# Kernel optimization log

Hardware: AMD Instinct MI355X
Metric: run time of the kernel (lower is better)

Reference implementation:

```python
import jax, jax.numpy as jnp
import numpy as np

B, H, S, D = 4, 16, 1024, 64

def setup_inputs() -> dict:
    key = jax.random.key(0)
    kq, kk, kv, kb, km = jax.random.split(key, 5)
    return {
        "q": jax.random.normal(kq, (B, H, S, D), dtype=jnp.float32),
        "k": jax.random.normal(kk, (B, H, S, D), dtype=jnp.float32),
        "v": jax.random.normal(kv, (B, H, S, D), dtype=jnp.float32),
        "add_attn": jax.random.normal(kb, (B, 1, S, S), dtype=jnp.float32),
        "mask": jax.random.randint(km, (B, 1, 1, S), 0, 2, dtype=jnp.int32),
    }

def reference(q, k, v, add_attn, mask):
    d_emb = q.shape[-1]
    scale = 1.0 / jnp.sqrt(jnp.float32(d_emb)).astype(q.dtype)
    # scores: [B,H,Sq,Sk]
    attn = jnp.einsum('bhqd,bhkd->bhqk', q * scale, k)
    attn = attn + add_attn
    attn = jnp.where(mask == 0, jnp.asarray(-1e9, attn.dtype), attn)
    attn = jax.nn.softmax(attn, axis=-1)  # dropout with p=0 is identity
    output = jnp.einsum('bhqk,bhkd->bhqd', attn, v)
    return (output, attn)
```

## Files before the change

kernel.cpp:

```cpp
#include <hip/hip_runtime.h>
#include <math.h>

#define BB 4
#define HH 16
#define SS 1024
#define DD 64
#define QT 16
#define NKW 4
#define KPW 256
#define HPB 4
#define PTL 264
#define OSTR 68

typedef __attribute__((ext_vector_type(8))) short bf16x8;
typedef __attribute__((ext_vector_type(4))) float f32x4;
typedef __attribute__((ext_vector_type(4))) int   i32x4;

static __device__ inline unsigned short f2bf(float f) {
    unsigned int u = __float_as_uint(f);
    u += 0x7fff + ((u >> 16) & 1);
    return (unsigned short)(u >> 16);
}

__global__ __launch_bounds__(256) void convert_qk(const float* __restrict__ q,
                                                  const float* __restrict__ k,
                                                  unsigned short* __restrict__ qb,
                                                  unsigned short* __restrict__ kb) {
    const int idx = blockIdx.x * 256 + threadIdx.x;
    float4 qv = ((const float4*)q)[idx];
    float4 kv = ((const float4*)k)[idx];
    ushort4 qo = make_ushort4(f2bf(qv.x), f2bf(qv.y), f2bf(qv.z), f2bf(qv.w));
    ushort4 ko = make_ushort4(f2bf(kv.x), f2bf(kv.y), f2bf(kv.z), f2bf(kv.w));
    ((ushort4*)qb)[idx] = qo;
    ((ushort4*)kb)[idx] = ko;
}

__global__ __launch_bounds__(256) void transpose_v(const float* __restrict__ v,
                                                   unsigned short* __restrict__ vt) {
    __shared__ unsigned short t[DD][258];
    const int bh = blockIdx.y;
    const int k0 = blockIdx.x * 256;
    const float* vb = v + ((size_t)bh * SS + k0) * DD;
#pragma unroll
    for (int j = 0; j < 16; ++j) {
        const int f   = j * 256 + threadIdx.x;
        const int row = f >> 4;
        const int d4  = (f & 15) << 2;
        float4 x = ((const float4*)vb)[f];
        t[d4 + 0][row] = f2bf(x.x);
        t[d4 + 1][row] = f2bf(x.y);
        t[d4 + 2][row] = f2bf(x.z);
        t[d4 + 3][row] = f2bf(x.w);
    }
    __syncthreads();
    unsigned short* vo = vt + (size_t)bh * DD * SS + k0;
#pragma unroll
    for (int j = 0; j < 8; ++j) {
        const int f  = j * 256 + threadIdx.x;
        const int d  = f >> 5;
        const int k8 = (f & 31) << 3;
        const unsigned int* lp = (const unsigned int*)&t[d][k8];
        uint4 w;
        w.x = lp[0]; w.y = lp[1]; w.z = lp[2]; w.w = lp[3];
        *(uint4*)(vo + (size_t)d * SS + k8) = w;
    }
}

__global__ __launch_bounds__(256, 2) void attn_mfma(
    const unsigned short* __restrict__ qb,
    const unsigned short* __restrict__ kb,
    const unsigned short* __restrict__ vtb,
    const float* __restrict__ add_attn,
    const int*   __restrict__ mask,
    float* __restrict__ out,
    float* __restrict__ attn_out)
{
    const int P    = blockIdx.x;
    const int xcd  = P & 7;
    const int slot = P >> 3;
    const int hg   = slot & 3;
    const int g    = ((slot >> 2) << 3) | xcd;
    const int qt   = g & 63;
    const int b    = g >> 6;

    const int tid  = threadIdx.x;
    const int wave = tid >> 6;
    const int lane = tid & 63;
    const int col  = lane & 15;
    const int quad = lane >> 4;

    __shared__ unsigned short p_tile[NKW][QT][PTL];
    __shared__ float red_m[NKW][QT];
    __shared__ float red_l[NKW][QT];
    float* o_w = (float*)&p_tile[wave][0][0];

    const int q0  = qt * QT;
    const int wk0 = wave * KPW;

    const float* brow = add_attn + ((size_t)b * SS + q0 + col) * SS;
    const int*   mrow = mask + b * SS;
    float br[16][4];
#pragma unroll
    for (int t = 0; t < 16; ++t) {
        const int kof = wk0 + t * 16 + quad * 4;
        const f32x4 bv = *(const f32x4*)(brow + kof);
        const i32x4 mv = *(const i32x4*)(mrow + kof);
#pragma unroll
        for (int r = 0; r < 4; ++r)
            br[t][r] = mv[r] ? bv[r] : -1e9f;
    }

    for (int hi = 0; hi < HPB; ++hi) {
        const int bh = b * HH + hg * HPB + hi;

        const unsigned short* qrow = qb + ((size_t)bh * SS + q0 + col) * DD + quad * 8;
        const bf16x8 bq0 = *(const bf16x8*)(qrow);
        const bf16x8 bq1 = *(const bf16x8*)(qrow + 32);

        const unsigned short* kbb = kb + (size_t)bh * SS * DD;

        float s[16][4];
#pragma unroll
        for (int t = 0; t < 16; ++t) {
            const unsigned short* kr = kbb + (size_t)(wk0 + t * 16 + col) * DD + quad * 8;
            bf16x8 ak0 = *(const bf16x8*)(kr);
            bf16x8 ak1 = *(const bf16x8*)(kr + 32);
            f32x4 acc = {0.f, 0.f, 0.f, 0.f};
            acc = __builtin_amdgcn_mfma_f32_16x16x32_bf16(ak0, bq0, acc, 0, 0, 0);
            acc = __builtin_amdgcn_mfma_f32_16x16x32_bf16(ak1, bq1, acc, 0, 0, 0);
#pragma unroll
            for (int r = 0; r < 4; ++r)
                s[t][r] = acc[r] * 0.125f + br[t][r];
        }

        float m = s[0][0];
#pragma unroll
        for (int t = 0; t < 16; ++t)
#pragma unroll
            for (int r = 0; r < 4; ++r) m = fmaxf(m, s[t][r]);
        m = fmaxf(m, __shfl_xor(m, 16));
        m = fmaxf(m, __shfl_xor(m, 32));

        float l = 0.f;
#pragma unroll
        for (int t = 0; t < 16; ++t)
#pragma unroll
            for (int r = 0; r < 4; ++r) {
                float e = __expf(s[t][r] - m);
                s[t][r] = e;
                l += e;
            }
        l += __shfl_xor(l, 16);
        l += __shfl_xor(l, 32);

        if (quad == 0) { red_m[wave][col] = m; red_l[wave][col] = l; }
        __syncthreads();

        const float m0 = red_m[0][col], m1 = red_m[1][col];
        const float m2 = red_m[2][col], m3 = red_m[3][col];
        const float gm = fmaxf(fmaxf(m0, m1), fmaxf(m2, m3));
        const float L  = red_l[0][col] * __expf(m0 - gm) +
                         red_l[1][col] * __expf(m1 - gm) +
                         red_l[2][col] * __expf(m2 - gm) +
                         red_l[3][col] * __expf(m3 - gm);
        const float sc = __expf(m - gm) / L;

        float* arow = attn_out + ((size_t)bh * SS + q0 + col) * SS + wk0;
#pragma unroll
        for (int t = 0; t < 16; ++t) {
            f32x4 pv;
            ushort4 pk;
#pragma unroll
            for (int r = 0; r < 4; ++r) {
                float p = s[t][r] * sc;
                pv[r] = p;
                ((unsigned short*)&pk)[r] = f2bf(p);
            }
            *(f32x4*)(arow + t * 16 + quad * 4) = pv;
            *(ushort4*)&p_tile[wave][col][t * 16 + quad * 4] = pk;
        }

        const unsigned short* vt = vtb + (size_t)bh * DD * SS;
        f32x4 oacc[4];
#pragma unroll
        for (int dc = 0; dc < 4; ++dc) oacc[dc] = (f32x4){0.f, 0.f, 0.f, 0.f};
#pragma unroll
        for (int c = 0; c < 8; ++c) {
            bf16x8 ap = *(const bf16x8*)(&p_tile[wave][col][c * 32 + quad * 8]);
#pragma unroll
            for (int dc = 0; dc < 4; ++dc) {
                const unsigned short* vr =
                    vt + (size_t)(dc * 16 + col) * SS + wk0 + c * 32 + quad * 8;
                bf16x8 av = *(const bf16x8*)(vr);
                oacc[dc] = __builtin_amdgcn_mfma_f32_16x16x32_bf16(av, ap, oacc[dc], 0, 0, 0);
            }
        }
#pragma unroll
        for (int dc = 0; dc < 4; ++dc)
            *(f32x4*)(o_w + col * OSTR + dc * 16 + quad * 4) = oacc[dc];
        __syncthreads();

        {
            const int qr = tid >> 4;
            const int d0 = (tid & 15) << 2;
            const float* ob = (const float*)&p_tile[0][0][0];
            const int ws = QT * PTL / 2;
            f32x4 a0 = *(const f32x4*)(ob + 0 * ws + qr * OSTR + d0);
            f32x4 a1 = *(const f32x4*)(ob + 1 * ws + qr * OSTR + d0);
            f32x4 a2 = *(const f32x4*)(ob + 2 * ws + qr * OSTR + d0);
            f32x4 a3 = *(const f32x4*)(ob + 3 * ws + qr * OSTR + d0);
            f32x4 o4 = a0 + a1 + a2 + a3;
            *(f32x4*)(out + ((size_t)bh * SS + q0 + qr) * DD + d0) = o4;
        }
        __syncthreads();
    }
}

extern "C" void kernel_launch(void* const* d_in, const int* in_sizes, int n_in,
                              void* d_out, int out_size, void* d_ws, size_t ws_size,
                              hipStream_t stream) {
    const float* q        = (const float*)d_in[0];
    const float* k        = (const float*)d_in[1];
    const float* v        = (const float*)d_in[2];
    const float* add_attn = (const float*)d_in[3];
    const int*   mask     = (const int*)d_in[4];

    float* out      = (float*)d_out;
    float* attn_out = (float*)d_out + (size_t)BB * HH * SS * DD;

    const size_t nelem = (size_t)BB * HH * SS * DD;
    unsigned short* qb  = (unsigned short*)d_ws;
    unsigned short* kbb = qb + nelem;
    unsigned short* vtb = kbb + nelem;

    convert_qk<<<dim3(nelem / 4 / 256), dim3(256), 0, stream>>>(q, k, qb, kbb);
    transpose_v<<<dim3(SS / 256, BB * HH), dim3(256), 0, stream>>>(v, vtb);

    attn_mfma<<<dim3(SS / QT * (HH / HPB) * BB), dim3(256), 0, stream>>>(
        qb, kbb, vtb, add_attn, mask, out, attn_out);
}
```

Measured before the change: 465.9 us.

## Replace 4-wave split-K blocks with single-wave two-pass online-softmax attention

Each block becomes a single wavefront that owns one head and one 16-row query tile across the full key length. A first pass computes the row max and sum with an online softmax, and a second pass recomputes QK^T to write the normalized probabilities and accumulate PV. This removes the cross-wave LDS reductions and __syncthreads barriers, and raises the block count to 4096 with an XCD-aware remap. In exchange, QK^T is computed twice, and the bias and mask are read twice per head instead of being reused across four heads held in registers.

```diff
diff --git a/kernel.cpp b/kernel.cpp
--- a/kernel.cpp
+++ b/kernel.cpp
@@ -6,11 +6,7 @@
 #define SS 1024
 #define DD 64
 #define QT 16
-#define NKW 4
-#define KPW 256
-#define HPB 4
 #define PTL 264
-#define OSTR 68
 
 typedef __attribute__((ext_vector_type(8))) short bf16x8;
 typedef __attribute__((ext_vector_type(4))) float f32x4;
@@ -66,7 +62,7 @@
     }
 }
 
-__global__ __launch_bounds__(256, 2) void attn_mfma(
+__global__ __launch_bounds__(64) void attn_1wave(
     const unsigned short* __restrict__ qb,
     const unsigned short* __restrict__ kb,
     const unsigned short* __restrict__ vtb,
@@ -75,145 +71,113 @@
     float* __restrict__ out,
     float* __restrict__ attn_out)
 {
-    const int P    = blockIdx.x;
-    const int xcd  = P & 7;
-    const int slot = P >> 3;
-    const int hg   = slot & 3;
-    const int g    = ((slot >> 2) << 3) | xcd;
-    const int qt   = g & 63;
-    const int b    = g >> 6;
-
-    const int tid  = threadIdx.x;
-    const int wave = tid >> 6;
-    const int lane = tid & 63;
+    const int P       = blockIdx.x;
+    const int logical = ((P & 7) << 9) | (P >> 3);
+    const int h  = logical & 15;
+    const int g  = logical >> 4;
+    const int qt = g & 63;
+    const int b  = g >> 6;
+    const int bh = b * HH + h;
+
+    const int lane = threadIdx.x;
     const int col  = lane & 15;
     const int quad = lane >> 4;
 
-    __shared__ unsigned short p_tile[NKW][QT][PTL];
-    __shared__ float red_m[NKW][QT];
-    __shared__ float red_l[NKW][QT];
-    float* o_w = (float*)&p_tile[wave][0][0];
-
-    const int q0  = qt * QT;
-    const int wk0 = wave * KPW;
-
+    __shared__ unsigned short p_tile[QT][PTL];
+
+    const int q0 = qt * QT;
+
+    const unsigned short* qrow = qb + ((size_t)bh * SS + q0 + col) * DD + quad * 8;
+    const bf16x8 bq0 = *(const bf16x8*)(qrow);
+    const bf16x8 bq1 = *(const bf16x8*)(qrow + 32);
+
+    const unsigned short* kbb = kb + (size_t)bh * SS * DD;
     const float* brow = add_attn + ((size_t)b * SS + q0 + col) * SS;
     const int*   mrow = mask + b * SS;
-    float br[16][4];
-#pragma unroll
-    for (int t = 0; t < 16; ++t) {
-        const int kof = wk0 + t * 16 + quad * 4;
+
+    float m = -3.0e38f, l = 0.0f;
+#pragma unroll 4
+    for (int t = 0; t < 64; ++t) {
+        const unsigned short* kr = kbb + (size_t)(t * 16 + col) * DD + quad * 8;
+        bf16x8 ak0 = *(const bf16x8*)(kr);
+        bf16x8 ak1 = *(const bf16x8*)(kr + 32);
+        f32x4 acc = {0.f, 0.f, 0.f, 0.f};
+        acc = __builtin_amdgcn_mfma_f32_16x16x32_bf16(ak0, bq0, acc, 0, 0, 0);
+        acc = __builtin_amdgcn_mfma_f32_16x16x32_bf16(ak1, bq1, acc, 0, 0, 0);
+        const int kof = t * 16 + quad * 4;
         const f32x4 bv = *(const f32x4*)(brow + kof);
         const i32x4 mv = *(const i32x4*)(mrow + kof);
-#pragma unroll
-        for (int r = 0; r < 4; ++r)
-            br[t][r] = mv[r] ? bv[r] : -1e9f;
-    }
-
-    for (int hi = 0; hi < HPB; ++hi) {
-        const int bh = b * HH + hg * HPB + hi;
-
-        const unsigned short* qrow = qb + ((size_t)bh * SS + q0 + col) * DD + quad * 8;
-        const bf16x8 bq0 = *(const bf16x8*)(qrow);
-        const bf16x8 bq1 = *(const bf16x8*)(qrow + 32);
-
-        const unsigned short* kbb = kb + (size_t)bh * SS * DD;
-
-        float s[16][4];
-#pragma unroll
-        for (int t = 0; t < 16; ++t) {
-            const unsigned short* kr = kbb + (size_t)(wk0 + t * 16 + col) * DD + quad * 8;
+        const float s0 = mv[0] ? acc[0] * 0.125f + bv[0] : -1e9f;
+        const float s1 = mv[1] ? acc[1] * 0.125f + bv[1] : -1e9f;
+        const float s2 = mv[2] ? acc[2] * 0.125f + bv[2] : -1e9f;
+        const float s3 = mv[3] ? acc[3] * 0.125f + bv[3] : -1e9f;
+        const float tm = fmaxf(fmaxf(s0, s1), fmaxf(s2, s3));
+        const float nm = fmaxf(m, tm);
+        l = l * __expf(m - nm) + __expf(s0 - nm) + __expf(s1 - nm)
+                               + __expf(s2 - nm) + __expf(s3 - nm);
+        m = nm;
+    }
+    {
+        float om = __shfl_xor(m, 16), ol = __shfl_xor(l, 16);
+        float nm = fmaxf(m, om);
+        l = l * __expf(m - nm) + ol * __expf(om - nm);
+        m = nm;
+        om = __shfl_xor(m, 32); ol = __shfl_xor(l, 32);
+        nm = fmaxf(m, om);
+        l = l * __expf(m - nm) + ol * __expf(om - nm);
+        m = nm;
+    }
+    const float inv = 1.0f / l;
+
+    const unsigned short* vt = vtb + (size_t)bh * DD * SS;
+    float* arow = attn_out + ((size_t)bh * SS + q0 + col) * SS;
+    f32x4 oacc[4];
+#pragma unroll
+    for (int dc = 0; dc < 4; ++dc) oacc[dc] = (f32x4){0.f, 0.f, 0.f, 0.f};
+
+    for (int ck = 0; ck < 4; ++ck) {
+        const int k0 = ck * 256;
+#pragma unroll
+        for (int tt = 0; tt < 16; ++tt) {
+            const int t = ck * 16 + tt;
+            const unsigned short* kr = kbb + (size_t)(t * 16 + col) * DD + quad * 8;
             bf16x8 ak0 = *(const bf16x8*)(kr);
             bf16x8 ak1 = *(const bf16x8*)(kr + 32);
             f32x4 acc = {0.f, 0.f, 0.f, 0.f};
             acc = __builtin_amdgcn_mfma_f32_16x16x32_bf16(ak0, bq0, acc, 0, 0, 0);
             acc = __builtin_amdgcn_mfma_f32_16x16x32_bf16(ak1, bq1, acc, 0, 0, 0);
-#pragma unroll
-            for (int r = 0; r < 4; ++r)
-                s[t][r] = acc[r] * 0.125f + br[t][r];
-        }
-
-        float m = s[0][0];
-#pragma unroll
-        for (int t = 0; t < 16; ++t)
-#pragma unroll
-            for (int r = 0; r < 4; ++r) m = fmaxf(m, s[t][r]);
-        m = fmaxf(m, __shfl_xor(m, 16));
-        m = fmaxf(m, __shfl_xor(m, 32));
-
-        float l = 0.f;
-#pragma unroll
-        for (int t = 0; t < 16; ++t)
-#pragma unroll
-            for (int r = 0; r < 4; ++r) {
-                float e = __expf(s[t][r] - m);
-                s[t][r] = e;
-                l += e;
-            }
-        l += __shfl_xor(l, 16);
-        l += __shfl_xor(l, 32);
-
-        if (quad == 0) { red_m[wave][col] = m; red_l[wave][col] = l; }
-        __syncthreads();
-
-        const float m0 = red_m[0][col], m1 = red_m[1][col];
-        const float m2 = red_m[2][col], m3 = red_m[3][col];
-        const float gm = fmaxf(fmaxf(m0, m1), fmaxf(m2, m3));
-        const float L  = red_l[0][col] * __expf(m0 - gm) +
-                         red_l[1][col] * __expf(m1 - gm) +
-                         red_l[2][col] * __expf(m2 - gm) +
-                         red_l[3][col] * __expf(m3 - gm);
-        const float sc = __expf(m - gm) / L;
-
-        float* arow = attn_out + ((size_t)bh * SS + q0 + col) * SS + wk0;
-#pragma unroll
-        for (int t = 0; t < 16; ++t) {
+            const int kof = t * 16 + quad * 4;
+            const f32x4 bv = *(const f32x4*)(brow + kof);
+            const i32x4 mv = *(const i32x4*)(mrow + kof);
             f32x4 pv;
             ushort4 pk;
 #pragma unroll
             for (int r = 0; r < 4; ++r) {
-                float p = s[t][r] * sc;
+                const float s = mv[r] ? acc[r] * 0.125f + bv[r] : -1e9f;
+                const float p = __expf(s - m) * inv;
                 pv[r] = p;
                 ((unsigned short*)&pk)[r] = f2bf(p);
             }
-            *(f32x4*)(arow + t * 16 + quad * 4) = pv;
-            *(ushort4*)&p_tile[wave][col][t * 16 + quad * 4] = pk;
+            *(f32x4*)(arow + kof) = pv;
+            *(ushort4*)&p_tile[col][tt * 16 + quad * 4] = pk;
         }
-
-        const unsigned short* vt = vtb + (size_t)bh * DD * SS;
-        f32x4 oacc[4];
-#pragma unroll
-        for (int dc = 0; dc < 4; ++dc) oacc[dc] = (f32x4){0.f, 0.f, 0.f, 0.f};
+        asm volatile("s_waitcnt lgkmcnt(0)" ::: "memory");
 #pragma unroll
         for (int c = 0; c < 8; ++c) {
-            bf16x8 ap = *(const bf16x8*)(&p_tile[wave][col][c * 32 + quad * 8]);
+            bf16x8 ap = *(const bf16x8*)&p_tile[col][c * 32 + quad * 8];
 #pragma unroll
             for (int dc = 0; dc < 4; ++dc) {
                 const unsigned short* vr =
-                    vt + (size_t)(dc * 16 + col) * SS + wk0 + c * 32 + quad * 8;
+                    vt + (size_t)(dc * 16 + col) * SS + k0 + c * 32 + quad * 8;
                 bf16x8 av = *(const bf16x8*)(vr);
                 oacc[dc] = __builtin_amdgcn_mfma_f32_16x16x32_bf16(av, ap, oacc[dc], 0, 0, 0);
             }
         }
-#pragma unroll
-        for (int dc = 0; dc < 4; ++dc)
-            *(f32x4*)(o_w + col * OSTR + dc * 16 + quad * 4) = oacc[dc];
-        __syncthreads();
-
-        {
-            const int qr = tid >> 4;
-            const int d0 = (tid & 15) << 2;
-            const float* ob = (const float*)&p_tile[0][0][0];
-            const int ws = QT * PTL / 2;
-            f32x4 a0 = *(const f32x4*)(ob + 0 * ws + qr * OSTR + d0);
-            f32x4 a1 = *(const f32x4*)(ob + 1 * ws + qr * OSTR + d0);
-            f32x4 a2 = *(const f32x4*)(ob + 2 * ws + qr * OSTR + d0);
-            f32x4 a3 = *(const f32x4*)(ob + 3 * ws + qr * OSTR + d0);
-            f32x4 o4 = a0 + a1 + a2 + a3;
-            *(f32x4*)(out + ((size_t)bh * SS + q0 + qr) * DD + d0) = o4;
-        }
-        __syncthreads();
-    }
+    }
+
+#pragma unroll
+    for (int dc = 0; dc < 4; ++dc)
+        *(f32x4*)(out + ((size_t)bh * SS + q0 + col) * DD + dc * 16 + quad * 4) = oacc[dc];
 }
 
 extern "C" void kernel_launch(void* const* d_in, const int* in_sizes, int n_in,
@@ -236,6 +200,6 @@
     convert_qk<<<dim3(nelem / 4 / 256), dim3(256), 0, stream>>>(q, k, qb, kbb);
     transpose_v<<<dim3(SS / 256, BB * HH), dim3(256), 0, stream>>>(v, vtb);
 
-    attn_mfma<<<dim3(SS / QT * (HH / HPB) * BB), dim3(256), 0, stream>>>(
+    attn_1wave<<<dim3(BB * HH * (SS / QT)), dim3(64), 0, stream>>>(
         qb, kbb, vtb, add_attn, mask, out, attn_out);
 }
```

After: 580.7 us. 1.25x slower.
